# Kernel tuning notes

Hardware: AMD Instinct MI355X
Metric: run time of the kernel (lower is better)

The kernel has to match this reference:

```python
import jax, jax.numpy as jnp
import numpy as np

N_NODES = 100000
N_EDGES = 1600000
D_IN = 64
D_OUT = 64
CLAMP = -10000.0  # scatter_'max' post-clamp threshold from the source


def setup_inputs() -> dict:
    key = jax.random.key(0)
    k1, k2, k3, k4, k5 = jax.random.split(key, 5)
    n_feat = jax.random.normal(k1, (N_NODES, D_IN), dtype=jnp.float32)
    src = jax.random.randint(k2, (N_EDGES,), 0, N_NODES, dtype=jnp.int64)
    dst = jax.random.randint(k3, (N_EDGES,), 0, N_NODES, dtype=jnp.int64)
    W = jax.random.normal(k4, (2 * D_IN, D_OUT), dtype=jnp.float32) / np.sqrt(2 * D_IN)
    b = jax.random.normal(k5, (D_OUT,), dtype=jnp.float32) * 0.01
    return {"n_feat": n_feat, "src": src, "dst": dst, "W": W, "b": b}


def reference(n_feat, src, dst, W, b):
    # gather endpoint features and form relative messages: [E, d]
    diff = n_feat[src] - n_feat[dst]
    # scatter-max aggregate onto destination nodes: [N, d]
    agg = jax.ops.segment_max(diff, dst, num_segments=n_feat.shape[0])
    # torch_scatter fills empty slots with lowest value; source clamps out<-10000 to 0
    agg = jnp.where(agg < CLAMP, 0.0, agg)
    # concat original + aggregated, then MLP = Linear + ReLU: [N, 2d] @ [2d, out]
    h = jnp.concatenate([n_feat, agg], axis=1)
    return jax.nn.relu(h @ W + b)
```

## Files before the change

kernel.cpp:

```cpp
#include <hip/hip_runtime.h>
#include <hip/hip_bf16.h>

#define D 64
#define CLAMP_V -10000.0f
#define SBSHIFT 9
#define SBN 512
#define MAXSB 256
#define HCHUNK 4096
#define SCHUNK 4096

typedef __bf16 bf16x4 __attribute__((ext_vector_type(4)));
typedef __bf16 bf16x8 __attribute__((ext_vector_type(8)));
typedef float floatx4 __attribute__((ext_vector_type(4)));
typedef unsigned short u16x2 __attribute__((ext_vector_type(2)));
typedef short s16x2 __attribute__((ext_vector_type(2)));

__device__ __forceinline__ unsigned pkmax(unsigned a, unsigned b) {
    u16x2 r = __builtin_elementwise_max(__builtin_bit_cast(u16x2, a),
                                        __builtin_bit_cast(u16x2, b));
    return __builtin_bit_cast(unsigned, r);
}
__device__ __forceinline__ uint4 pkmax4(uint4 a, uint4 b) {
    uint4 r;
    r.x = pkmax(a.x, b.x); r.y = pkmax(a.y, b.y);
    r.z = pkmax(a.z, b.z); r.w = pkmax(a.w, b.w);
    return r;
}
__device__ __forceinline__ unsigned pk_ord_encode(unsigned g) {
    s16x2 t = __builtin_bit_cast(s16x2, g) >> 15;
    unsigned m = __builtin_bit_cast(unsigned, t) & 0x7FFF7FFFu;
    return g ^ (m | 0x80008000u);
}
__device__ __forceinline__ unsigned pk_ord_decode(unsigned e) {
    s16x2 t = __builtin_bit_cast(s16x2, e) >> 15;
    unsigned m = (~__builtin_bit_cast(unsigned, t)) & 0x7FFF7FFFu;
    return e ^ (m | 0x80008000u);
}
__device__ __forceinline__ unsigned seg_finish(unsigned enc, unsigned xr) {
    unsigned raw = pk_ord_decode(enc);
    float v0 = __uint_as_float(raw << 16);
    float v1 = __uint_as_float(raw & 0xFFFF0000u);
    float x0 = __uint_as_float(xr << 16);
    float x1 = __uint_as_float(xr & 0xFFFF0000u);
    float r0 = v0 - x0; r0 = (r0 >= CLAMP_V) ? r0 : 0.0f;
    float r1 = v1 - x1; r1 = (r1 >= CLAMP_V) ? r1 : 0.0f;
    __bf16 b0 = (__bf16)r0, b1 = (__bf16)r1;
    return ((unsigned)__builtin_bit_cast(unsigned short, b1) << 16)
         |  (unsigned)__builtin_bit_cast(unsigned short, b0);
}

__global__ __launch_bounds__(256) void prep_kernel(
        const float* __restrict__ nf, __bf16* __restrict__ nf16,
        unsigned* __restrict__ nfenc, int n4,
        const int* __restrict__ dst, unsigned* __restrict__ ghist,
        int nE, int nbSB,
        const float* __restrict__ W, __bf16* __restrict__ wfrag,
        int histBlocks, int wBlock) {
    __shared__ unsigned h[MAXSB];
    int blk = blockIdx.x, t = threadIdx.x;
    int i = blk * 256 + t;
    if (i < n4) {
        float4 v = ((const float4*)nf)[i];
        __bf16 b0 = (__bf16)v.x, b1 = (__bf16)v.y;
        __bf16 b2 = (__bf16)v.z, b3 = (__bf16)v.w;
        bf16x4 o = { b0, b1, b2, b3 };
        ((bf16x4*)nf16)[i] = o;
        unsigned d0 = ((unsigned)__builtin_bit_cast(unsigned short, b1) << 16)
                    |  (unsigned)__builtin_bit_cast(unsigned short, b0);
        unsigned d1 = ((unsigned)__builtin_bit_cast(unsigned short, b3) << 16)
                    |  (unsigned)__builtin_bit_cast(unsigned short, b2);
        uint2 e; e.x = pk_ord_encode(d0); e.y = pk_ord_encode(d1);
        ((uint2*)nfenc)[i] = e;
    }
    if (blk < histBlocks) {
        if (t < MAXSB) h[t] = 0;
        __syncthreads();
        int e0 = blk * HCHUNK;
        int ec = nE - e0; if (ec > HCHUNK) ec = HCHUNK;
        for (int k = t; k < ec; k += 256) atomicAdd(&h[dst[e0 + k] >> SBSHIFT], 1u);
        __syncthreads();
        if (t < (unsigned)nbSB && h[t]) atomicAdd(&ghist[t], h[t]);
    }
    if (blk == wBlock) {
        for (int idx = t; idx < 2 * D * D; idx += 256) {
            int k = idx >> 6, n = idx & 63;
            int ks = k >> 5, r = k & 31, quad = r >> 3, j = r & 7;
            int c = n >> 4, l16 = n & 15;
            int fidx = (((ks * 4 + c) * 64) + quad * 16 + l16) * 8 + j;
            wfrag[fidx] = (__bf16)W[idx];
        }
    }
}

__global__ __launch_bounds__(256) void scan_sb(
        const unsigned* __restrict__ ghist, unsigned* __restrict__ base,
        unsigned* __restrict__ cursor, int nbSB) {
    __shared__ unsigned ts[256];
    int t = threadIdx.x;
    unsigned v = (t < nbSB) ? ghist[t] : 0u;
    ts[t] = v; __syncthreads();
    for (int off = 1; off < 256; off <<= 1) {
        unsigned x = (t >= off) ? ts[t - off] : 0u;
        __syncthreads();
        ts[t] += x;
        __syncthreads();
    }
    if (t < nbSB) {
        unsigned ex = ts[t] - v;
        base[t] = ex; cursor[t] = ex;
        if (t == nbSB - 1) base[nbSB] = ts[t];
    }
}

__global__ __launch_bounds__(256) void sb_scatter(
        const int* __restrict__ src, const int* __restrict__ dst,
        unsigned* __restrict__ cursor, unsigned* __restrict__ packed,
        int nE, int nbSB) {
    __shared__ unsigned cop[MAXSB];
    __shared__ unsigned short lb16[MAXSB];
    __shared__ unsigned gbase[MAXSB];
    __shared__ unsigned payload[SCHUNK];
    __shared__ unsigned char sbid[SCHUNK];
    __shared__ unsigned ts[256];
    int t = threadIdx.x;
    int e0 = blockIdx.x * SCHUNK;
    int ec = nE - e0; if (ec > SCHUNK) ec = SCHUNK;

    if (t < MAXSB) cop[t] = 0;
    __syncthreads();
    for (int i = t; i < ec; i += 256)
        atomicAdd(&cop[dst[e0 + i] >> SBSHIFT], 1u);
    __syncthreads();
    unsigned c = (t < nbSB) ? (cop[t] & 0xFFFFu) : 0u;
    ts[t] = c; __syncthreads();
    for (int o = 1; o < 256; o <<= 1) {
        unsigned x = (t >= o) ? ts[t - o] : 0u;
        __syncthreads();
        ts[t] += x;
        __syncthreads();
    }
    if (t < nbSB) {
        lb16[t] = (unsigned short)(ts[t] - c);
        if (c) gbase[t] = atomicAdd(&cursor[t], c);
    }
    __syncthreads();
    for (int i = t; i < ec; i += 256) {
        int e = e0 + i;
        int d = dst[e];
        int b = d >> SBSHIFT;
        unsigned p = atomicAdd(&cop[b], 0x10000u) >> 16;
        unsigned pos = (unsigned)lb16[b] + p;
        payload[pos] = ((unsigned)(d & (SBN - 1)) << 17) | (unsigned)src[e];
        sbid[pos] = (unsigned char)b;
    }
    __syncthreads();
    for (int i = t; i < ec; i += 256) {
        unsigned b = sbid[i];
        packed[gbase[b] + ((unsigned)i - (unsigned)lb16[b])] = payload[i];
    }
}

__global__ __launch_bounds__(256) void sb_sort(
        const unsigned* __restrict__ packed1, const unsigned* __restrict__ base,
        unsigned* __restrict__ packed2, unsigned* __restrict__ nodestart,
        int nN) {
    __shared__ unsigned cnt[SBN];
    __shared__ unsigned ts[256];
    int sb = blockIdx.x, t = threadIdx.x;
    unsigned beg = base[sb], end = base[sb + 1];
    cnt[2 * t] = 0; cnt[2 * t + 1] = 0;
    __syncthreads();
    for (unsigned i = beg + t; i < end; i += 256)
        atomicAdd(&cnt[packed1[i] >> 17], 1u);
    __syncthreads();
    unsigned a = cnt[2 * t], b = cnt[2 * t + 1], s = a + b;
    ts[t] = s; __syncthreads();
    for (int o = 1; o < 256; o <<= 1) {
        unsigned x = (t >= o) ? ts[t - o] : 0u;
        __syncthreads();
        ts[t] += x;
        __syncthreads();
    }
    unsigned ex = ts[t] - s;
    cnt[2 * t] = ex; cnt[2 * t + 1] = ex + a;
    int n0 = sb * SBN;
    if (n0 + 2 * t     <= nN) nodestart[n0 + 2 * t]     = beg + ex;
    if (n0 + 2 * t + 1 <= nN) nodestart[n0 + 2 * t + 1] = beg + ex + a;
    __syncthreads();
    for (unsigned i = beg + t; i < end; i += 256) {
        unsigned e = packed1[i];
        unsigned p = atomicAdd(&cnt[e >> 17], 1u);
        packed2[beg + p] = e & 0x1FFFFu;
    }
}

__global__ __launch_bounds__(256) void seg_direct(
        const uint4* __restrict__ enc4,
        const uint4* __restrict__ nfu4,
        const unsigned* __restrict__ packed2,
        const unsigned* __restrict__ nodestart,
        uint4* __restrict__ agg4,
        int nN) {
    int t = threadIdx.x;
    int ln = t & 63;
    int grp = ln >> 3;
    int col = ln & 7;
    int n = blockIdx.x * 32 + (t >> 6) * 8 + grp;
    if (n >= nN) return;
    unsigned rb = nodestart[n], re = nodestart[n + 1];
    unsigned deg = re - rb;
    const uint4* ec = enc4 + col;
    uint4 a0 = {0,0,0,0}, a1 = {0,0,0,0}, a2 = {0,0,0,0}, a3 = {0,0,0,0};
    unsigned i = 0;
    for (; i + 4 <= deg; i += 4) {
        unsigned e0 = packed2[rb + i];
        unsigned e1 = packed2[rb + i + 1];
        unsigned e2 = packed2[rb + i + 2];
        unsigned e3 = packed2[rb + i + 3];
        uint4 g0 = ec[(size_t)e0 * 8];
        uint4 g1 = ec[(size_t)e1 * 8];
        uint4 g2 = ec[(size_t)e2 * 8];
        uint4 g3 = ec[(size_t)e3 * 8];
        a0 = pkmax4(a0, g0);
        a1 = pkmax4(a1, g1);
        a2 = pkmax4(a2, g2);
        a3 = pkmax4(a3, g3);
    }
    for (; i < deg; ++i) {
        unsigned e0 = packed2[rb + i];
        a0 = pkmax4(a0, ec[(size_t)e0 * 8]);
    }
    uint4 m = pkmax4(pkmax4(a0, a1), pkmax4(a2, a3));
    uint4 xr = nfu4[(size_t)n * 8 + col];
    uint4 o;
    o.x = seg_finish(m.x, xr.x);
    o.y = seg_finish(m.y, xr.y);
    o.z = seg_finish(m.z, xr.z);
    o.w = seg_finish(m.w, xr.w);
    agg4[(size_t)n * 8 + col] = o;
}

__global__ __launch_bounds__(256) void node_mlp_mfma(
        const __bf16* __restrict__ nf16,
        const __bf16* __restrict__ agg16,
        float* __restrict__ out,
        const __bf16* __restrict__ wfrag,
        const float* __restrict__ bias,
        int nTiles, int nN) {
    int lane = threadIdx.x & 63;
    int quad = lane >> 4;
    int l16  = lane & 15;
    int waveGlobal = blockIdx.x * 4 + (threadIdx.x >> 6);
    int nWaves = gridDim.x * 4;

    bf16x8 bfrag[4][4];
    #pragma unroll
    for (int c = 0; c < 4; ++c)
        #pragma unroll
        for (int ks = 0; ks < 4; ++ks)
            bfrag[c][ks] = *(const bf16x8*)(wfrag + ((size_t)((ks * 4 + c) * 64 + lane)) * 8);
    float bv[4];
    #pragma unroll
    for (int c = 0; c < 4; ++c) bv[c] = bias[c * 16 + l16];

    for (int t = waveGlobal; t < nTiles; t += nWaves) {
        int n0 = t * 16;
        int rowA = n0 + l16;
        if (rowA >= nN) rowA = nN - 1;
        const __bf16* nfr = nf16  + (size_t)rowA * D;
        const __bf16* agr = agg16 + (size_t)rowA * D;

        floatx4 acc[4] = {{0,0,0,0},{0,0,0,0},{0,0,0,0},{0,0,0,0}};
        #pragma unroll
        for (int ks = 0; ks < 4; ++ks) {
            const __bf16* p = (ks < 2) ? (nfr + ks * 32 + quad * 8)
                                       : (agr + (ks - 2) * 32 + quad * 8);
            bf16x8 a = *(const bf16x8*)p;
            #pragma unroll
            for (int c = 0; c < 4; ++c)
                acc[c] = __builtin_amdgcn_mfma_f32_16x16x32_bf16(
                             a, bfrag[c][ks], acc[c], 0, 0, 0);
        }
        #pragma unroll
        for (int r = 0; r < 4; ++r) {
            int row = n0 + quad * 4 + r;
            if (row < nN) {
                #pragma unroll
                for (int c = 0; c < 4; ++c) {
                    float vv = acc[c][r] + bv[c];
                    out[(size_t)row * D + c * 16 + l16] = fmaxf(vv, 0.0f);
                }
            }
        }
    }
}

extern "C" void kernel_launch(void* const* d_in, const int* in_sizes, int n_in,
                              void* d_out, int out_size, void* d_ws, size_t ws_size,
                              hipStream_t stream) {
    const float* nf  = (const float*)d_in[0];
    const int*   src = (const int*)d_in[1];
    const int*   dst = (const int*)d_in[2];
    const float* W   = (const float*)d_in[3];
    const float* b   = (const float*)d_in[4];
    float* out = (float*)d_out;

    int nN = in_sizes[0] / D;
    int nE = in_sizes[1];
    int nbSB = (nN + SBN - 1) / SBN;

    char* wsb = (char*)d_ws;
    size_t nfB  = (((size_t)nN * D * 2) + 255) & ~(size_t)255;
    size_t pkB  = (((size_t)nE * 4)     + 255) & ~(size_t)255;
    __bf16*   nf16   = (__bf16*)wsb;
    __bf16*   agg16  = (__bf16*)(wsb + nfB);
    unsigned* packed1 = (unsigned*)(wsb + 2 * nfB);
    unsigned* ghist  = (unsigned*)(wsb + 2 * nfB + pkB);
    unsigned* base   = (unsigned*)(wsb + 2 * nfB + pkB + 4 * MAXSB);
    unsigned* cursor = (unsigned*)(wsb + 2 * nfB + pkB + 4 * MAXSB + 4 * (MAXSB + 2));
    __bf16*   wfrag  = (__bf16*)(wsb + 2 * nfB + pkB + 4 * MAXSB + 8 * (MAXSB + 2));
    unsigned* nodestart = (unsigned*)(wsb + 2 * nfB + pkB + 4 * MAXSB
                                      + 8 * (MAXSB + 2) + 32768);
    unsigned* packed2 = (unsigned*)d_out;
    unsigned* nfenc   = (unsigned*)((char*)d_out + pkB);

    hipMemsetAsync(ghist, 0, (size_t)nbSB * 4, stream);

    int n4 = nN * D / 4;
    int convBlocks = (n4 + 255) / 256;
    int histBlocks = (nE + HCHUNK - 1) / HCHUNK;
    int gridPrep = convBlocks > histBlocks ? convBlocks : histBlocks;
    prep_kernel<<<gridPrep, 256, 0, stream>>>(nf, nf16, nfenc, n4, dst, ghist,
                                              nE, nbSB, W, wfrag,
                                              histBlocks, gridPrep - 1);

    scan_sb<<<1, 256, 0, stream>>>(ghist, base, cursor, nbSB);

    int nbS = (nE + SCHUNK - 1) / SCHUNK;
    sb_scatter<<<nbS, 256, 0, stream>>>(src, dst, cursor, packed1, nE, nbSB);

    sb_sort<<<nbSB, 256, 0, stream>>>(packed1, base, packed2, nodestart, nN);

    int segBlocks = (nN + 31) / 32;
    seg_direct<<<segBlocks, 256, 0, stream>>>(
        (const uint4*)nfenc, (const uint4*)nf16, packed2, nodestart,
        (uint4*)agg16, nN);

    int nTiles = (nN + 15) / 16;
    node_mlp_mfma<<<768, 256, 0, stream>>>(nf16, agg16, out, wfrag, b, nTiles, nN);
}
```

Before: 195.8 us.

## Degree-sort nodes within seg_direct blocks to balance per-wave gather work

The segment-max kernel now handles 128 nodes per 512-thread block. It counting-sorts those nodes by in-degree in shared memory, so each wave processes nodes of similar degree, which reduces divergence from a wave waiting on its slowest 8-lane group. It also reads the node's own feature from the encoded array and decodes it, instead of loading a separate bf16 copy. The cost is extra shared-memory sorting with several barriers per block, and the sorted mapping breaks the contiguity of the output writes.

```diff
diff --git a/kernel.cpp b/kernel.cpp
--- a/kernel.cpp
+++ b/kernel.cpp
@@ -8,6 +8,8 @@
 #define MAXSB 256
 #define HCHUNK 4096
 #define SCHUNK 4096
+#define SEG_NODES 128
+#define SEG_THREADS 512
 
 typedef __bf16 bf16x4 __attribute__((ext_vector_type(4)));
 typedef __bf16 bf16x8 __attribute__((ext_vector_type(8)));
@@ -36,8 +38,9 @@
     unsigned m = (~__builtin_bit_cast(unsigned, t)) & 0x7FFF7FFFu;
     return e ^ (m | 0x80008000u);
 }
-__device__ __forceinline__ unsigned seg_finish(unsigned enc, unsigned xr) {
-    unsigned raw = pk_ord_decode(enc);
+__device__ __forceinline__ unsigned seg_finish2(unsigned encm, unsigned encs) {
+    unsigned raw = pk_ord_decode(encm);
+    unsigned xr  = pk_ord_decode(encs);
     float v0 = __uint_as_float(raw << 16);
     float v1 = __uint_as_float(raw & 0xFFFF0000u);
     float x0 = __uint_as_float(xr << 16);
@@ -194,50 +197,87 @@
     }
 }
 
-__global__ __launch_bounds__(256) void seg_direct(
+__global__ __launch_bounds__(SEG_THREADS) void seg_direct(
         const uint4* __restrict__ enc4,
-        const uint4* __restrict__ nfu4,
         const unsigned* __restrict__ packed2,
         const unsigned* __restrict__ nodestart,
         uint4* __restrict__ agg4,
         int nN) {
+    __shared__ unsigned nsh[SEG_NODES + 1];
+    __shared__ unsigned hist[128];
+    __shared__ unsigned cur[128];
+    __shared__ unsigned short sorted[SEG_NODES];
     int t = threadIdx.x;
-    int ln = t & 63;
+    int n0 = blockIdx.x * SEG_NODES;
+    if (t < SEG_NODES + 1) {
+        int idx = n0 + t; if (idx > nN) idx = nN;
+        nsh[t] = nodestart[idx];
+    }
+    if (t < 128) hist[t] = 0;
+    __syncthreads();
+    unsigned bin = 0;
+    if (t < SEG_NODES) {
+        unsigned dg = nsh[t + 1] - nsh[t];
+        bin = dg < 127u ? dg : 127u;
+        atomicAdd(&hist[bin], 1u);
+    }
+    __syncthreads();
+    unsigned myc = (t < 128) ? hist[t] : 0u;
+    for (int o = 1; o < 128; o <<= 1) {
+        unsigned x = 0;
+        if (t < 128 && t >= o) x = hist[t - o];
+        __syncthreads();
+        if (t < 128) hist[t] += x;
+        __syncthreads();
+    }
+    if (t < 128) cur[t] = hist[t] - myc;
+    __syncthreads();
+    if (t < SEG_NODES) {
+        unsigned pos = atomicAdd(&cur[bin], 1u);
+        sorted[pos] = (unsigned short)t;
+    }
+    __syncthreads();
+    int wv = t >> 6, ln = t & 63;
     int grp = ln >> 3;
     int col = ln & 7;
-    int n = blockIdx.x * 32 + (t >> 6) * 8 + grp;
-    if (n >= nN) return;
-    unsigned rb = nodestart[n], re = nodestart[n + 1];
-    unsigned deg = re - rb;
     const uint4* ec = enc4 + col;
-    uint4 a0 = {0,0,0,0}, a1 = {0,0,0,0}, a2 = {0,0,0,0}, a3 = {0,0,0,0};
-    unsigned i = 0;
-    for (; i + 4 <= deg; i += 4) {
-        unsigned e0 = packed2[rb + i];
-        unsigned e1 = packed2[rb + i + 1];
-        unsigned e2 = packed2[rb + i + 2];
-        unsigned e3 = packed2[rb + i + 3];
-        uint4 g0 = ec[(size_t)e0 * 8];
-        uint4 g1 = ec[(size_t)e1 * 8];
-        uint4 g2 = ec[(size_t)e2 * 8];
-        uint4 g3 = ec[(size_t)e3 * 8];
-        a0 = pkmax4(a0, g0);
-        a1 = pkmax4(a1, g1);
-        a2 = pkmax4(a2, g2);
-        a3 = pkmax4(a3, g3);
-    }
-    for (; i < deg; ++i) {
-        unsigned e0 = packed2[rb + i];
-        a0 = pkmax4(a0, ec[(size_t)e0 * 8]);
-    }
-    uint4 m = pkmax4(pkmax4(a0, a1), pkmax4(a2, a3));
-    uint4 xr = nfu4[(size_t)n * 8 + col];
-    uint4 o;
-    o.x = seg_finish(m.x, xr.x);
-    o.y = seg_finish(m.y, xr.y);
-    o.z = seg_finish(m.z, xr.z);
-    o.w = seg_finish(m.w, xr.w);
-    agg4[(size_t)n * 8 + col] = o;
+    #pragma unroll 1
+    for (int k = 0; k < SEG_NODES / 64; ++k) {
+        int lid = sorted[(k * 8 + wv) * 8 + grp];
+        int n = n0 + lid;
+        unsigned rb = nsh[lid], re = nsh[lid + 1];
+        unsigned deg = re - rb;
+        uint4 a0 = {0,0,0,0}, a1 = {0,0,0,0}, a2 = {0,0,0,0}, a3 = {0,0,0,0};
+        unsigned i = 0;
+        for (; i + 4 <= deg; i += 4) {
+            unsigned e0 = packed2[rb + i];
+            unsigned e1 = packed2[rb + i + 1];
+            unsigned e2 = packed2[rb + i + 2];
+            unsigned e3 = packed2[rb + i + 3];
+            uint4 g0 = ec[(size_t)e0 * 8];
+            uint4 g1 = ec[(size_t)e1 * 8];
+            uint4 g2 = ec[(size_t)e2 * 8];
+            uint4 g3 = ec[(size_t)e3 * 8];
+            a0 = pkmax4(a0, g0);
+            a1 = pkmax4(a1, g1);
+            a2 = pkmax4(a2, g2);
+            a3 = pkmax4(a3, g3);
+        }
+        for (; i < deg; ++i) {
+            unsigned e0 = packed2[rb + i];
+            a0 = pkmax4(a0, ec[(size_t)e0 * 8]);
+        }
+        uint4 m = pkmax4(pkmax4(a0, a1), pkmax4(a2, a3));
+        if (n < nN) {
+            uint4 es = ec[(size_t)n * 8];
+            uint4 o;
+            o.x = seg_finish2(m.x, es.x);
+            o.y = seg_finish2(m.y, es.y);
+            o.z = seg_finish2(m.z, es.z);
+            o.w = seg_finish2(m.w, es.w);
+            agg4[(size_t)n * 8 + col] = o;
+        }
+    }
 }
 
 __global__ __launch_bounds__(256) void node_mlp_mfma(
@@ -341,10 +381,9 @@
 
     sb_sort<<<nbSB, 256, 0, stream>>>(packed1, base, packed2, nodestart, nN);
 
-    int segBlocks = (nN + 31) / 32;
-    seg_direct<<<segBlocks, 256, 0, stream>>>(
-        (const uint4*)nfenc, (const uint4*)nf16, packed2, nodestart,
-        (uint4*)agg16, nN);
+    int segBlocks = (nN + SEG_NODES - 1) / SEG_NODES;
+    seg_direct<<<segBlocks, SEG_THREADS, 0, stream>>>(
+        (const uint4*)nfenc, packed2, nodestart, (uint4*)agg16, nN);
 
     int nTiles = (nN + 15) / 16;
     node_mlp_mfma<<<768, 256, 0, stream>>>(nf16, agg16, out, wfrag, b, nTiles, nN);
```

New measurement: 198.3 us. About the same (+1.3%).
